# Kernel optimization log

Measured on AMD Instinct MI355X. Metric: run time of the kernel, lower is better.

## Reference

```python
import jax, jax.numpy as jnp
import numpy as np

R = 3            # corr_radius
KK = 2 * R + 1   # 7
K = KK * KK      # 49 support points
LEVELS = 4       # corr_levels


def _offsets():
    # matches get_support_points: meshgrid over [-r, r] applied to (x, y)
    d = jnp.arange(-R, R + 1, dtype=jnp.float32)
    ox, oy = jnp.meshgrid(d, d, indexing='ij')
    return jnp.stack([ox, oy], -1).reshape(K, 2)


def _bilinear(fmap_flat, fidx, x, y):
    """Bilinear sample with zero padding (grid_sample align_corners=True semantics
    for pixel-space coords). fmap_flat: (F,H,W,D); fidx int (...); x,y float (...).
    Returns (..., D)."""
    Hs, Ws = fmap_flat.shape[1], fmap_flat.shape[2]
    x0 = jnp.floor(x); y0 = jnp.floor(y)
    tx = x - x0; ty = y - y0

    def tap(xi, yi, w):
        valid = (xi >= 0) & (xi <= Ws - 1) & (yi >= 0) & (yi <= Hs - 1)
        xc = jnp.clip(xi, 0, Ws - 1).astype(jnp.int32)
        yc = jnp.clip(yi, 0, Hs - 1).astype(jnp.int32)
        return fmap_flat[fidx, yc, xc] * (w * valid)[..., None]

    return (tap(x0, y0, (1 - tx) * (1 - ty)) + tap(x0 + 1, y0, tx * (1 - ty))
            + tap(x0, y0 + 1, (1 - tx) * ty) + tap(x0 + 1, y0 + 1, tx * ty))


def reference(fmaps, coords, queried_coords, queried_frames, w1, b1, w2, b2):
    """Multi-scale correlation-volume pipeline of CoTrackerThreeOffline:
    L2-normalize fmaps, build avg-pool pyramid, sample 7x7 track-support feats
    at query frames, sample 7x7 correlation feats at current coords per frame,
    einsum 49x49 corr volume, corr_mlp (2401->384 GELU ->256), concat levels."""
    B, T, D, H, W = fmaps.shape
    N = coords.shape[2]
    fm = jnp.transpose(fmaps, (0, 1, 3, 4, 2))  # (B,T,H,W,D)
    fm = fm / jnp.sqrt(jnp.maximum(jnp.sum(fm * fm, -1, keepdims=True), 1e-12))
    offs = _offsets()
    fidx_t = jnp.arange(B * T).reshape(B, T, 1, 1)          # frame index per (b,t)
    fq = (jnp.arange(B)[:, None] * T + queried_frames)[..., None]  # (B,N,1)
    embs = []
    for lvl in range(LEVELS):
        Hs, Ws = fm.shape[2], fm.shape[3]
        fm_flat = fm.reshape(B * T, Hs, Ws, D)
        # track support features at the query frame (7x7 around query coord)
        qc = queried_coords / (2.0 ** lvl)                   # (B,N,2)
        px = qc[..., 0:1] + offs[:, 0]; py = qc[..., 1:2] + offs[:, 1]  # (B,N,K)
        tf = _bilinear(fm_flat, fq, px, py)                  # (B,N,K,D)
        # correlation features around current coords for every frame
        cl = coords / (2.0 ** lvl)                           # (B,T,N,2)
        cx = cl[..., 0:1] + offs[:, 0]; cy = cl[..., 1:2] + offs[:, 1]  # (B,T,N,K)
        cf = _bilinear(fm_flat, fidx_t, cx, cy)              # (B,T,N,K,D)
        # 49x49 correlation volume then corr_mlp
        vol = jnp.einsum('btnkc,bnlc->btnkl', cf, tf).reshape(B * T * N, K * K)
        emb = jax.nn.gelu(vol @ w1 + b1, approximate=False) @ w2 + b2
        embs.append(emb.reshape(B, T, N, -1))
        if lvl < LEVELS - 1:  # avg_pool2d k=2 s=2
            fm = fm.reshape(B, T, Hs // 2, 2, Ws // 2, 2, D).mean(axis=(3, 5))
    return jnp.concatenate(embs, -1)  # (B,T,N,4*256)


def setup_inputs() -> dict:
    key = jax.random.key(0)
    ks = jax.random.split(key, 6)
    B, T, D, H, W, N = 1, 24, 128, 96, 128, 256
    fmaps = jax.random.normal(ks[0], (B, T, D, H, W), jnp.float32)
    scale_xy = jnp.array([W - 1.0, H - 1.0], jnp.float32)
    queried_coords = jax.random.uniform(ks[1], (B, N, 2), jnp.float32) * scale_xy
    queried_frames = jax.random.randint(ks[2], (B, N), 0, T)
    coords = jax.random.uniform(ks[3], (B, T, N, 2), jnp.float32) * scale_xy
    w1 = jax.random.normal(ks[4], (K * K, 384), jnp.float32) * 0.02
    b1 = jnp.zeros((384,), jnp.float32)
    w2 = jax.random.normal(ks[5], (384, 256), jnp.float32) * 0.02
    b2 = jnp.zeros((256,), jnp.float32)
    return dict(fmaps=fmaps, coords=coords, queried_coords=queried_coords,
                queried_frames=queried_frames, w1=w1, b1=b1, w2=w2, b2=b2)
```

## Files before the change

kernel.cpp:

```cpp
#include <hip/hip_runtime.h>
#include <hip/hip_bf16.h>
#include <stdint.h>

#define T_   24
#define D_   128
#define H_   96
#define W_   128
#define N_   256
#define KP   49
#define K2   3136
#define H1   384
#define OUTC 256
#define MTOT (4 * T_ * N_)

#define PAD  8
#define GSTR 68

typedef __attribute__((ext_vector_type(8))) __bf16 bf16x8;
typedef __attribute__((ext_vector_type(4))) float f32x4;

typedef __attribute__((address_space(3))) unsigned int lds_u32;
typedef const __attribute__((address_space(1))) unsigned int g_u32;
#define GLOAD16(g, l) __builtin_amdgcn_global_load_lds((g_u32*)(g), (lds_u32*)(l), 16, 0, 0)

__device__ inline float bf2f(unsigned short u) {
    union { unsigned int i; float f; } v; v.i = ((unsigned int)u) << 16; return v.f;
}
__device__ inline unsigned short f2bf(float f) {
    union { float f; unsigned int i; } v; v.f = f;
    unsigned int i = v.i;
    return (unsigned short)((i + 0x7FFFu + ((i >> 16) & 1u)) >> 16);
}
__device__ inline unsigned int cvtpk(float lo, float hi) {
    unsigned int r;
    asm("v_cvt_pk_bf16_f32 %0, %1, %2" : "=v"(r) : "v"(lo), "v"(hi));
    return r;
}

__global__ __launch_bounds__(256) void k_padzero(uint4* __restrict__ fm,
                                                 int Hs, int Ws) {
    int PW = Ws + 2 * PAD, PH = Hs + 2 * PAD;
    size_t upf = (size_t)PH * PW * 16;
    size_t total = upf * T_;
    for (size_t idx = (size_t)blockIdx.x * 256 + threadIdx.x; idx < total;
         idx += (size_t)gridDim.x * 256) {
        size_t p = idx >> 4;
        size_t pf = p % ((size_t)PH * PW);
        int y = (int)(pf / PW), x = (int)(pf % PW);
        if (y < PAD || y >= Hs + PAD || x < PAD || x >= Ws + PAD) {
            uint4 z = {0u, 0u, 0u, 0u};
            fm[idx] = z;
        }
    }
}

__global__ __launch_bounds__(256) void k_w1t(const float* __restrict__ w1,
                                             unsigned short* __restrict__ w1t) {
    __shared__ float tile[64][65];
    int bn = blockIdx.x, k = blockIdx.y;
    int tid = threadIdx.x;
    int nl = tid & 63, q = tid >> 6;
#pragma unroll
    for (int i = 0; i < 16; ++i) {
        int l = q * 16 + i;
        float v = (l < KP) ? w1[((size_t)k * KP + l) * H1 + bn * 64 + nl] : 0.f;
        tile[l][nl] = v;
    }
    __syncthreads();
#pragma unroll
    for (int i = 0; i < 16; ++i) {
        int nn = q * 16 + i;
        w1t[(size_t)(bn * 64 + nn) * K2 + k * 64 + nl] = f2bf(tile[nl][nn]);
    }
}
__global__ __launch_bounds__(256) void k_w2t(const float* __restrict__ w2,
                                             unsigned short* __restrict__ w2t) {
    int idx = blockIdx.x * 256 + threadIdx.x;
    if (idx >= OUTC * H1) return;
    int j = idx / H1, k = idx % H1;
    w2t[idx] = f2bf(w2[(size_t)k * OUTC + j]);
}

#define PW0 (W_ + 2 * PAD)
#define FR0 ((size_t)(H_ + 2 * PAD) * PW0 * D_)
__global__ __launch_bounds__(256) void k_normalize(const float* __restrict__ fmaps,
                                                   unsigned short* __restrict__ fm0i) {
    int bid = blockIdx.x;
    int t = bid / H_, h = bid % H_;
    int tid = threadIdx.x;
    __shared__ float tile[64 * 129];
    __shared__ float ssumP[64][4];
    __shared__ float rs[64];
    const float* base = fmaps + (size_t)t * D_ * H_ * W_ + (size_t)h * W_;
    unsigned short* orow = fm0i + (size_t)t * FR0 + (size_t)h * (PW0 * D_);
    for (int wt = 0; wt < 2; ++wt) {
        int wl = tid & 63, dg = tid >> 6;
        float ss = 0.f;
        for (int i = 0; i < 32; ++i) {
            int d = dg * 32 + i;
            float v = base[(size_t)d * (H_ * W_) + wt * 64 + wl];
            tile[wl * 129 + d] = v;
            ss += v * v;
        }
        ssumP[wl][dg] = ss;
        __syncthreads();
        if (tid < 64)
            rs[tid] = rsqrtf(fmaxf(ssumP[tid][0] + ssumP[tid][1] + ssumP[tid][2] + ssumP[tid][3], 1e-12f));
        __syncthreads();
        int c = tid & 63, rg = tid >> 6;
        for (int i = 0; i < 16; ++i) {
            int wll = rg * 16 + i;
            float r = rs[wll];
            float v0 = tile[wll * 129 + c * 2] * r;
            float v1 = tile[wll * 129 + c * 2 + 1] * r;
            *(unsigned int*)(orow + (size_t)(wt * 64 + wll) * D_ + c * 2) = cvtpk(v0, v1);
        }
        __syncthreads();
    }
}

__global__ __launch_bounds__(256) void k_pool(const unsigned short* __restrict__ ini,
                                              unsigned short* __restrict__ outi,
                                              int Hs, int Ws) {
    int Ho = Hs >> 1, Wo = Ws >> 1;
    int PWi = Ws + 2 * PAD, PWo = Wo + 2 * PAD;
    size_t FRi = (size_t)(Hs + 2 * PAD) * PWi * D_;
    size_t FRo = (size_t)(Ho + 2 * PAD) * PWo * D_;
    size_t total = (size_t)T_ * Ho * Wo * (D_ / 4);
    size_t idx = (size_t)blockIdx.x * 256 + threadIdx.x;
    if (idx >= total) return;
    int d4 = idx & 31;
    size_t p = idx >> 5;
    int x = (int)(p % Wo); p /= Wo;
    int y = (int)(p % Ho); int t = (int)(p / Ho);
    const unsigned short* b0 = ini + (size_t)t * FRi + ((size_t)(2 * y) * PWi + 2 * x) * D_ + d4 * 4;
    const unsigned short* b1r = b0 + (size_t)PWi * D_;
    float acc[4] = {0.f, 0.f, 0.f, 0.f};
#pragma unroll
    for (int j = 0; j < 2; ++j) {
        const unsigned short* bb = j ? b1r : b0;
#pragma unroll
        for (int i = 0; i < 2; ++i) {
            const unsigned short* q = bb + i * D_;
#pragma unroll
            for (int c = 0; c < 4; ++c) acc[c] += bf2f(q[c]);
        }
    }
    unsigned short* o = outi + (size_t)t * FRo + ((size_t)y * PWo + x) * D_ + d4 * 4;
#pragma unroll
    for (int c = 0; c < 4; ++c) o[c] = f2bf(acc[c] * 0.25f);
}

__device__ inline float2 bilin2p(const unsigned short* __restrict__ fb, int PW,
                                 float px, float py, int lane) {
    float x0f = floorf(px), y0f = floorf(py);
    float tx = px - x0f, ty = py - y0f;
    int x0 = (int)x0f, y0 = (int)y0f;
    float acc0 = 0.f, acc1 = 0.f;
#pragma unroll
    for (int dy = 0; dy < 2; ++dy) {
#pragma unroll
        for (int dx = 0; dx < 2; ++dx) {
            long xi = x0 + dx, yi = y0 + dy;
            float w = (dx ? tx : 1.f - tx) * (dy ? ty : 1.f - ty);
            unsigned int pk = *(const unsigned int*)(fb + (yi * PW + xi) * D_ + lane * 2);
            acc0 += w * bf2f((unsigned short)(pk & 0xffffu));
            acc1 += w * bf2f((unsigned short)(pk >> 16));
        }
    }
    return {acc0, acc1};
}

__global__ __launch_bounds__(256) void k_tf(const unsigned short* __restrict__ f0,
                                            const unsigned short* __restrict__ f1,
                                            const unsigned short* __restrict__ f2,
                                            const unsigned short* __restrict__ f3,
                                            const float* __restrict__ qcoords,
                                            const int* __restrict__ qframes,
                                            unsigned short* __restrict__ tfg) {
    int n = blockIdx.x, lvl = blockIdx.y;
    const unsigned short* fmi = lvl == 0 ? f0 : lvl == 1 ? f1 : lvl == 2 ? f2 : f3;
    int Hs = H_ >> lvl, Ws = W_ >> lvl;
    int PW = Ws + 2 * PAD;
    size_t FR = (size_t)(Hs + 2 * PAD) * PW * D_;
    float inv = 1.0f / (float)(1 << lvl);
    int wid = threadIdx.x >> 6, lane = threadIdx.x & 63;
    int fidx = qframes[n];
    float qx = qcoords[n * 2 + 0] * inv, qy = qcoords[n * 2 + 1] * inv;
    const unsigned short* fb = fmi + (size_t)fidx * FR;
    unsigned short* orow = tfg + ((size_t)lvl * N_ + n) * (64 * D_);
    for (int k = wid; k < 64; k += 4) {
        float2 v = {0.f, 0.f};
        if (k < KP) {
            float px = qx + (float)(k / 7 - 3);
            float py = qy + (float)(k % 7 - 3);
            v = bilin2p(fb, PW, px, py, lane);
        }
        *(unsigned int*)(orow + k * D_ + lane * 2) = cvtpk(v.x, v.y);
    }
}

__global__ __launch_bounds__(256) void k_cfvol(const unsigned short* __restrict__ f0,
                                               const unsigned short* __restrict__ f1,
                                               const unsigned short* __restrict__ f2,
                                               const unsigned short* __restrict__ f3,
                                               const float* __restrict__ coords,
                                               const unsigned short* __restrict__ tfg,
                                               unsigned short* __restrict__ vol) {
    __shared__ unsigned char tfs[16384];
    __shared__ unsigned char Ps[16384];
    unsigned short* Gs = (unsigned short*)tfs;
    int n = blockIdx.x, t = blockIdx.y, lvl = blockIdx.z;
    const unsigned short* fmi = lvl == 0 ? f0 : lvl == 1 ? f1 : lvl == 2 ? f2 : f3;
    int Hs = H_ >> lvl, Ws = W_ >> lvl;
    int PW = Ws + 2 * PAD;
    size_t FR = (size_t)(Hs + 2 * PAD) * PW * D_;
    float inv = 1.0f / (float)(1 << lvl);
    int tid = threadIdx.x, wid = tid >> 6, lane = tid & 63;
    int l15 = lane & 15, hi = lane >> 4;

    float cx = coords[((size_t)t * N_ + n) * 2 + 0] * inv;
    float cy = coords[((size_t)t * N_ + n) * 2 + 1] * inv;
    float fx = floorf(cx), fy = floorf(cy);
    float tx = cx - fx, ty = cy - fy;
    long bx = (long)(int)fx - 3, by = (long)(int)fy - 3;
    const unsigned short* fb = fmi + (size_t)t * FR;
    const unsigned short* tfn = tfg + ((size_t)lvl * N_ + n) * (64 * D_);
#pragma unroll
    for (int i = 0; i < 4; ++i) {
        int rr = wid * 16 + i * 4 + hi;
        int u = l15 ^ (rr & 7);
        GLOAD16(tfn + rr * 128 + u * 8, tfs + (wid * 4 + i) * 1024);
    }
#pragma unroll
    for (int i = 0; i < 4; ++i) {
        int rr = wid * 16 + i * 4 + hi;
        int u = l15 ^ (rr & 7);
        GLOAD16(fb + ((by + (rr & 7)) * (long)PW + (bx + (rr >> 3))) * D_ + u * 8,
                Ps + (wid * 4 + i) * 1024);
    }
    asm volatile("s_waitcnt vmcnt(0)" ::: "memory");
    __builtin_amdgcn_s_barrier();
    f32x4 acc[4] = {f32x4{0,0,0,0}, f32x4{0,0,0,0}, f32x4{0,0,0,0}, f32x4{0,0,0,0}};
#pragma unroll
    for (int ks = 0; ks < 4; ++ks) {
        int colb = ks * 64 + hi * 16;
        int arow = wid * 16 + l15;
        bf16x8 a = *(const bf16x8*)(Ps + arow * 256 + (colb ^ ((arow & 7) << 4)));
#pragma unroll
        for (int ln = 0; ln < 4; ++ln) {
            int brow = ln * 16 + l15;
            bf16x8 b = *(const bf16x8*)(tfs + brow * 256 + (colb ^ ((brow & 7) << 4)));
            acc[ln] = __builtin_amdgcn_mfma_f32_16x16x32_bf16(a, b, acc[ln], 0, 0, 0);
        }
    }
    __syncthreads();
#pragma unroll
    for (int ln = 0; ln < 4; ++ln)
#pragma unroll
        for (int r = 0; r < 4; ++r)
            Gs[(wid * 16 + hi * 4 + r) * GSTR + ln * 16 + l15] =
                (unsigned short)cvtpk(acc[ln][r], acc[ln][r]);
    __syncthreads();
    unsigned int* vrow = (unsigned int*)(vol + (((size_t)lvl * T_ + t) * N_ + n) * K2);
    float w00 = (1.f - tx) * (1.f - ty), w01 = (1.f - tx) * ty;
    float w10 = tx * (1.f - ty), w11 = tx * ty;
    int lh = lane >> 5, ll = lane & 31;
#pragma unroll
    for (int it = 0; it < 7; ++it) {
        int k = it * 8 + wid * 2 + lh;
        if (k < KP) {
            int a0 = k / 7, b0 = k - a0 * 7;
            int g = a0 * 8 + b0;
            const unsigned short* gp = &Gs[g * GSTR + ll * 2];
            unsigned int u00 = *(const unsigned int*)(gp);
            unsigned int u01 = *(const unsigned int*)(gp + GSTR);
            unsigned int u10 = *(const unsigned int*)(gp + 8 * GSTR);
            unsigned int u11 = *(const unsigned int*)(gp + 9 * GSTR);
            float r0 = w00 * bf2f((unsigned short)u00) + w01 * bf2f((unsigned short)u01)
                     + w10 * bf2f((unsigned short)u10) + w11 * bf2f((unsigned short)u11);
            float r1 = w00 * bf2f((unsigned short)(u00 >> 16)) + w01 * bf2f((unsigned short)(u01 >> 16))
                     + w10 * bf2f((unsigned short)(u10 >> 16)) + w11 * bf2f((unsigned short)(u11 >> 16));
            vrow[k * 32 + ll] = cvtpk(r0, r1);
        }
    }
}

__global__ __launch_bounds__(512) void k_gemm1(const unsigned short* __restrict__ A,
                                               const unsigned short* __restrict__ Bt,
                                               const float* __restrict__ b1,
                                               unsigned short* __restrict__ Hout) {
    __shared__ unsigned char As[16384];
    __shared__ unsigned char Bs[16384];
    int bid = blockIdx.x;
    int swz = (bid & 7) * 72 + (bid >> 3);
    int bm = swz / 3, bn = swz % 3;
    int tid = threadIdx.x, lane = tid & 63;
    int wid = tid >> 6, wm = wid & 3, wn = wid >> 2;
    int l15 = lane & 15, hi = lane >> 4;
    f32x4 acc[2][4] = {};
    const unsigned short* Abase = A + (size_t)(bm * 128) * K2;
    const unsigned short* Bbase = Bt + (size_t)(bn * 128) * K2;
    for (int kt = 0; kt < K2 / 64; ++kt) {
#pragma unroll
        for (int q = 0; q < 2; ++q) {
            int e = (wid * 2 + q) * 64 + lane;
            int row = e >> 3, su = (e & 7) ^ (row & 7);
            GLOAD16(Abase + (size_t)row * K2 + kt * 64 + su * 8, As + (wid * 2 + q) * 1024);
        }
#pragma unroll
        for (int q = 0; q < 2; ++q) {
            int e = (wid * 2 + q) * 64 + lane;
            int row = e >> 3, su = (e & 7) ^ (row & 7);
            GLOAD16(Bbase + (size_t)row * K2 + kt * 64 + su * 8, Bs + (wid * 2 + q) * 1024);
        }
        __syncthreads();
#pragma unroll
        for (int ks = 0; ks < 2; ++ks) {
            int colb = ks * 64 + hi * 16;
            bf16x8 a[2], b[4];
#pragma unroll
            for (int km = 0; km < 2; ++km) {
                int arow = wm * 32 + km * 16 + l15;
                a[km] = *(const bf16x8*)(As + arow * 128 + (colb ^ ((arow & 7) << 4)));
            }
#pragma unroll
            for (int ln = 0; ln < 4; ++ln) {
                int brow = wn * 64 + ln * 16 + l15;
                b[ln] = *(const bf16x8*)(Bs + brow * 128 + (colb ^ ((brow & 7) << 4)));
            }
#pragma unroll
            for (int km = 0; km < 2; ++km)
#pragma unroll
                for (int ln = 0; ln < 4; ++ln)
                    acc[km][ln] = __builtin_amdgcn_mfma_f32_16x16x32_bf16(a[km], b[ln], acc[km][ln], 0, 0, 0);
        }
        __syncthreads();
    }
#pragma unroll
    for (int km = 0; km < 2; ++km)
#pragma unroll
        for (int ln = 0; ln < 4; ++ln)
#pragma unroll
            for (int r = 0; r < 4; ++r) {
                int row = bm * 128 + wm * 32 + km * 16 + hi * 4 + r;
                int col = bn * 128 + wn * 64 + ln * 16 + l15;
                float x = acc[km][ln][r] + b1[col];
                float g = 0.5f * x * (1.f + erff(x * 0.70710678118654752f));
                Hout[(size_t)row * H1 + col] = f2bf(g);
            }
}

__global__ __launch_bounds__(512) void k_gemm2(const unsigned short* __restrict__ A,
                                               const unsigned short* __restrict__ Bt,
                                               const float* __restrict__ b2,
                                               float* __restrict__ outp) {
    __shared__ unsigned char As[16384];
    __shared__ unsigned char Bs[16384];
    int bid = blockIdx.x;
    int swz = (bid & 7) * 48 + (bid >> 3);
    int bm = swz >> 1, bn = swz & 1;
    int tid = threadIdx.x, lane = tid & 63;
    int wid = tid >> 6, wm = wid & 3, wn = wid >> 2;
    int l15 = lane & 15, hi = lane >> 4;
    f32x4 acc[2][4] = {};
    const unsigned short* Abase = A + (size_t)(bm * 128) * H1;
    const unsigned short* Bbase = Bt + (size_t)(bn * 128) * H1;
    for (int kt = 0; kt < H1 / 64; ++kt) {
#pragma unroll
        for (int q = 0; q < 2; ++q) {
            int e = (wid * 2 + q) * 64 + lane;
            int row = e >> 3, su = (e & 7) ^ (row & 7);
            GLOAD16(Abase + (size_t)row * H1 + kt * 64 + su * 8, As + (wid * 2 + q) * 1024);
        }
#pragma unroll
        for (int q = 0; q < 2; ++q) {
            int e = (wid * 2 + q) * 64 + lane;
            int row = e >> 3, su = (e & 7) ^ (row & 7);
            GLOAD16(Bbase + (size_t)row * H1 + kt * 64 + su * 8, Bs + (wid * 2 + q) * 1024);
        }
        __syncthreads();
#pragma unroll
        for (int ks = 0; ks < 2; ++ks) {
            int colb = ks * 64 + hi * 16;
            bf16x8 a[2], b[4];
#pragma unroll
            for (int km = 0; km < 2; ++km) {
                int arow = wm * 32 + km * 16 + l15;
                a[km] = *(const bf16x8*)(As + arow * 128 + (colb ^ ((arow & 7) << 4)));
            }
#pragma unroll
            for (int ln = 0; ln < 4; ++ln) {
                int brow = wn * 64 + ln * 16 + l15;
                b[ln] = *(const bf16x8*)(Bs + brow * 128 + (colb ^ ((brow & 7) << 4)));
            }
#pragma unroll
            for (int km = 0; km < 2; ++km)
#pragma unroll
                for (int ln = 0; ln < 4; ++ln)
                    acc[km][ln] = __builtin_amdgcn_mfma_f32_16x16x32_bf16(a[km], b[ln], acc[km][ln], 0, 0, 0);
        }
        __syncthreads();
    }
#pragma unroll
    for (int km = 0; km < 2; ++km)
#pragma unroll
        for (int ln = 0; ln < 4; ++ln)
#pragma unroll
            for (int r = 0; r < 4; ++r) {
                int row = bm * 128 + wm * 32 + km * 16 + hi * 4 + r;
                int col = bn * 128 + wn * 64 + ln * 16 + l15;
                int lvl = row / (T_ * N_);
                int r2 = row - lvl * (T_ * N_);
                outp[(size_t)r2 * (4 * OUTC) + lvl * OUTC + col] = acc[km][ln][r] + b2[col];
            }
}

extern "C" void kernel_launch(void* const* d_in, const int* in_sizes, int n_in,
                              void* d_out, int out_size, void* d_ws, size_t ws_size,
                              hipStream_t stream) {
    const float* fmaps   = (const float*)d_in[0];
    const float* coords  = (const float*)d_in[1];
    const float* qcoords = (const float*)d_in[2];
    const int*   qframes = (const int*)d_in[3];
    const float* w1      = (const float*)d_in[4];
    const float* b1      = (const float*)d_in[5];
    const float* w2      = (const float*)d_in[6];
    const float* b2      = (const float*)d_in[7];
    float* outp = (float*)d_out;

    unsigned char* ws = (unsigned char*)d_ws;
    size_t off = 0;
    auto take = [&](size_t bytes) {
        unsigned char* p = ws + off;
        off += (bytes + 255) & ~(size_t)255;
        return p;
    };
    const int Hs[4] = {96, 48, 24, 12}, Wss[4] = {128, 64, 32, 16};
    unsigned short* fmraw[4];
    unsigned short* fmint[4];
    for (int l = 0; l < 4; ++l) {
        int PH = Hs[l] + 2 * PAD, PW = Wss[l] + 2 * PAD;
        fmraw[l] = (unsigned short*)take((size_t)T_ * PH * PW * D_ * 2);
        fmint[l] = fmraw[l] + ((size_t)PAD * PW + PAD) * D_;
    }
    unsigned short* tfg  = (unsigned short*)take((size_t)4 * N_ * 64 * D_ * 2);
    unsigned short* vol  = (unsigned short*)take((size_t)MTOT * K2 * 2);
    unsigned short* hbuf = (unsigned short*)take((size_t)MTOT * H1 * 2);
    unsigned short* w1t  = (unsigned short*)take((size_t)H1 * K2 * 2);
    unsigned short* w2t  = (unsigned short*)take((size_t)OUTC * H1 * 2);

    for (int l = 0; l < 4; ++l)
        hipLaunchKernelGGL(k_padzero, dim3(4096), dim3(256), 0, stream,
                           (uint4*)fmraw[l], Hs[l], Wss[l]);
    hipLaunchKernelGGL(k_w1t, dim3(6, 49), dim3(256), 0, stream, w1, w1t);
    hipLaunchKernelGGL(k_w2t, dim3((OUTC * H1 + 255) / 256), dim3(256), 0, stream, w2, w2t);
    hipLaunchKernelGGL(k_normalize, dim3(T_ * H_), dim3(256), 0, stream, fmaps, fmint[0]);
    hipLaunchKernelGGL(k_pool, dim3((T_ * 48 * 64 * 32 + 255) / 256), dim3(256), 0, stream,
                       fmint[0], fmint[1], 96, 128);
    hipLaunchKernelGGL(k_pool, dim3((T_ * 24 * 32 * 32 + 255) / 256), dim3(256), 0, stream,
                       fmint[1], fmint[2], 48, 64);
    hipLaunchKernelGGL(k_pool, dim3((T_ * 12 * 16 * 32 + 255) / 256), dim3(256), 0, stream,
                       fmint[2], fmint[3], 24, 32);

    hipLaunchKernelGGL(k_tf, dim3(N_, 4), dim3(256), 0, stream,
                       fmint[0], fmint[1], fmint[2], fmint[3], qcoords, qframes, tfg);
    hipLaunchKernelGGL(k_cfvol, dim3(N_, T_, 4), dim3(256), 0, stream,
                       fmint[0], fmint[1], fmint[2], fmint[3], coords, tfg, vol);
    hipLaunchKernelGGL(k_gemm1, dim3(576), dim3(512), 0, stream, vol, w1t, b1, hbuf);
    hipLaunchKernelGGL(k_gemm2, dim3(384), dim3(512), 0, stream, hbuf, w2t, b2, outp);
}
```

Before: 304.0 us.

## Double-buffer LDS tiles in gemm1 to overlap global loads with MFMA

Gives the first GEMM kernel two LDS buffers for A and B. The next K-tile is prefetched with global_load_lds while the current tile feeds the MFMAs, and explicit vmcnt waits plus raw barriers replace the two __syncthreads per iteration. This hides global-load latency behind compute at the cost of doubling LDS to 64KB per block, which may reduce occupancy.

```diff
diff --git a/kernel.cpp b/kernel.cpp
--- a/kernel.cpp
+++ b/kernel.cpp
@@ -290,8 +290,8 @@
                                                const unsigned short* __restrict__ Bt,
                                                const float* __restrict__ b1,
                                                unsigned short* __restrict__ Hout) {
-    __shared__ unsigned char As[16384];
-    __shared__ unsigned char Bs[16384];
+    __shared__ unsigned char As[2][16384];
+    __shared__ unsigned char Bs[2][16384];
     int bid = blockIdx.x;
     int swz = (bid & 7) * 72 + (bid >> 3);
     int bm = swz / 3, bn = swz % 3;
@@ -301,20 +301,32 @@
     f32x4 acc[2][4] = {};
     const unsigned short* Abase = A + (size_t)(bm * 128) * K2;
     const unsigned short* Bbase = Bt + (size_t)(bn * 128) * K2;
-    for (int kt = 0; kt < K2 / 64; ++kt) {
+    auto STAGE = [&](int kt, int buf) {
 #pragma unroll
         for (int q = 0; q < 2; ++q) {
             int e = (wid * 2 + q) * 64 + lane;
             int row = e >> 3, su = (e & 7) ^ (row & 7);
-            GLOAD16(Abase + (size_t)row * K2 + kt * 64 + su * 8, As + (wid * 2 + q) * 1024);
+            GLOAD16(Abase + (size_t)row * K2 + kt * 64 + su * 8, As[buf] + (wid * 2 + q) * 1024);
         }
 #pragma unroll
         for (int q = 0; q < 2; ++q) {
             int e = (wid * 2 + q) * 64 + lane;
             int row = e >> 3, su = (e & 7) ^ (row & 7);
-            GLOAD16(Bbase + (size_t)row * K2 + kt * 64 + su * 8, Bs + (wid * 2 + q) * 1024);
-        }
-        __syncthreads();
+            GLOAD16(Bbase + (size_t)row * K2 + kt * 64 + su * 8, Bs[buf] + (wid * 2 + q) * 1024);
+        }
+    };
+    const int KT = K2 / 64;
+    STAGE(0, 0);
+    for (int kt = 0; kt < KT; ++kt) {
+        int cur = kt & 1;
+        if (kt + 1 < KT) {
+            STAGE(kt + 1, cur ^ 1);
+            asm volatile("s_waitcnt vmcnt(4)" ::: "memory");
+        } else {
+            asm volatile("s_waitcnt vmcnt(0)" ::: "memory");
+        }
+        __builtin_amdgcn_s_barrier();
+        __builtin_amdgcn_sched_barrier(0);
 #pragma unroll
         for (int ks = 0; ks < 2; ++ks) {
             int colb = ks * 64 + hi * 16;
@@ -322,12 +334,12 @@
 #pragma unroll
             for (int km = 0; km < 2; ++km) {
                 int arow = wm * 32 + km * 16 + l15;
-                a[km] = *(const bf16x8*)(As + arow * 128 + (colb ^ ((arow & 7) << 4)));
+                a[km] = *(const bf16x8*)(As[cur] + arow * 128 + (colb ^ ((arow & 7) << 4)));
             }
 #pragma unroll
             for (int ln = 0; ln < 4; ++ln) {
                 int brow = wn * 64 + ln * 16 + l15;
-                b[ln] = *(const bf16x8*)(Bs + brow * 128 + (colb ^ ((brow & 7) << 4)));
+                b[ln] = *(const bf16x8*)(Bs[cur] + brow * 128 + (colb ^ ((brow & 7) << 4)));
             }
 #pragma unroll
             for (int km = 0; km < 2; ++km)
@@ -335,7 +347,10 @@
                 for (int ln = 0; ln < 4; ++ln)
                     acc[km][ln] = __builtin_amdgcn_mfma_f32_16x16x32_bf16(a[km], b[ln], acc[km][ln], 0, 0, 0);
         }
-        __syncthreads();
+        if (kt + 1 < KT) {
+            __builtin_amdgcn_sched_barrier(0);
+            __builtin_amdgcn_s_barrier();
+        }
     }
 #pragma unroll
     for (int km = 0; km < 2; ++km)
```

Measured after the change: 335.2 us. 1.1x slower.
